# Optimization experiments

Hardware: AMD Instinct MI355X
Metric: run time of the kernel (lower is better)

Reference implementation:

```python
import jax, jax.numpy as jnp
import numpy as np

N = 8192
IN_F = 256
OUT_F = 128
ALPHA = 0.2
NEG = -9000000000000000.0

def setup_inputs() -> dict:
    key = jax.random.key(0)
    k1, k2, k3, k4 = jax.random.split(key, 4)
    h = jax.random.normal(k1, (N, IN_F), dtype=jnp.float32)
    adj = jax.random.randint(k2, (N, N), 0, 2, dtype=jnp.int32)
    # xavier-uniform-like params
    limW = float(np.sqrt(6.0 / (IN_F + OUT_F)))
    W = jax.random.uniform(k3, (IN_F, OUT_F), minval=-limW, maxval=limW, dtype=jnp.float32)
    lima = float(np.sqrt(6.0 / (2 * OUT_F + 1)))
    a = jax.random.uniform(k4, (2 * OUT_F, 1), minval=-lima, maxval=lima, dtype=jnp.float32)
    return {"h": h, "adj": adj, "W": W, "a": a}

def reference(h, adj, W, a):
    Wh = h @ W  # [N, F]
    # e_ij = LeakyReLU(a1.Wh_i + a2.Wh_j) -- avoids [N,N,2F] intermediate
    a1 = a[:OUT_F, 0]  # [F]
    a2 = a[OUT_F:, 0]  # [F]
    f1 = Wh @ a1  # [N]
    f2 = Wh @ a2  # [N]
    e = jax.nn.leaky_relu(f1[:, None] + f2[None, :], negative_slope=ALPHA)  # [N,N]
    att = jnp.where(adj > 0, e, jnp.float32(NEG))
    att = jax.nn.softmax(att, axis=1)
    h_prime = att @ Wh  # [N, F]
    return h_prime
```

## Files before the change

kernel.cpp:

```cpp
#include <hip/hip_runtime.h>
#include <hip/hip_bf16.h>

#define N    8192
#define INF  256
#define OUTF 128
#define ALPHA 0.2f
#define JS   8
#define NTS  (N / JS / 32)

typedef __attribute__((ext_vector_type(8))) short bf16x8;
typedef __attribute__((ext_vector_type(4))) float f32x4;

__device__ __forceinline__ unsigned short f2bf(float x) {
    union { float f; unsigned u; } v; v.f = x;
    unsigned r = v.u + 0x7fff + ((v.u >> 16) & 1);
    return (unsigned short)(r >> 16);
}

__device__ __forceinline__ void gll16(const void* g, void* l) {
    __builtin_amdgcn_global_load_lds(
        (const __attribute__((address_space(1))) unsigned*)g,
        (__attribute__((address_space(3))) unsigned*)l, 16, 0, 0);
}

__global__ __launch_bounds__(256) void k01_prep(
        const int* __restrict__ adj, unsigned* __restrict__ bits,
        const float* __restrict__ h, const float* __restrict__ W,
        const float* __restrict__ a,
        unsigned short* __restrict__ WhTb, float* __restrict__ f1, float* __restrict__ f2) {
    __shared__ float hs[8][INF];
    const int t = threadIdx.x;

    if (blockIdx.x >= 1024) {
        const size_t g = (size_t)(blockIdx.x - 1024) * 256 + t;
        const int4* p = (const int4*)adj + g * 8;
        unsigned b = 0;
        #pragma unroll
        for (int u = 0; u < 8; ++u) {
            int4 v = p[u];
            b |= (v.x > 0 ? 1u : 0u) << (u * 4 + 0);
            b |= (v.y > 0 ? 1u : 0u) << (u * 4 + 1);
            b |= (v.z > 0 ? 1u : 0u) << (u * 4 + 2);
            b |= (v.w > 0 ? 1u : 0u) << (u * 4 + 3);
        }
        bits[g] = b;
        return;
    }

    const int i0 = blockIdx.x * 8;
    #pragma unroll
    for (int u = 0; u < 2; ++u) {
        int idx = u * 256 + t;
        int r   = idx >> 6;
        int kq  = idx & 63;
        *(float4*)&hs[r][kq * 4] = *(const float4*)(h + (size_t)(i0 + r) * INF + kq * 4);
    }
    __syncthreads();

    const int rg = t >> 5;
    const int ct = t & 31;
    float acc[4] = {0.f, 0.f, 0.f, 0.f};

    #pragma unroll 8
    for (int k = 0; k < INF; ++k) {
        float4 wv = *(const float4*)(W + (size_t)k * OUTF + ct * 4);
        float  hx = hs[rg][k];
        acc[0] += hx * wv.x; acc[1] += hx * wv.y;
        acc[2] += hx * wv.z; acc[3] += hx * wv.w;
    }

    const int r0 = i0 + rg;
    const int jb = r0 >> 5;
    const int jo = r0 & 31;
    #pragma unroll
    for (int cc = 0; cc < 4; ++cc)
        WhTb[(size_t)jb * 4096 + (ct * 4 + cc) * 32 + jo] = f2bf(acc[cc]);

    const float4 a1v = *(const float4*)(a + ct * 4);
    const float4 a2v = *(const float4*)(a + OUTF + ct * 4);
    float p1 = acc[0]*a1v.x + acc[1]*a1v.y + acc[2]*a1v.z + acc[3]*a1v.w;
    float p2 = acc[0]*a2v.x + acc[1]*a2v.y + acc[2]*a2v.z + acc[3]*a2v.w;
    #pragma unroll
    for (int off = 16; off > 0; off >>= 1) {
        p1 += __shfl_down(p1, off, 32);
        p2 += __shfl_down(p2, off, 32);
    }
    if (ct == 0) { f1[r0] = p1; f2[r0] = p2; }
}

__device__ __forceinline__ float pbit(float f1r, float fv, unsigned byte_,
                                      int u, float& dsum) {
    float s = f1r + fv;
    float e = fmaxf(s, ALPHA * s);
    float p = (byte_ & (1u << u)) ? __expf(e) : 0.f;
    dsum += p;
    return p;
}

#define K2SUB(WORD, PH, JT)                                                  \
    {                                                                        \
        if ((JT) + 1 < NTS) {                                                \
            const char* ws_ = (const char*)WhTb + (size_t)(tile0 + (JT) + 1) * 8192; \
            char* bd_ = (char*)&bsm[(PH) ^ 1][0];                            \
            gll16(ws_ + t * 16,        bd_ + wv * 1024 + 0);                 \
            gll16(ws_ + 4096 + t * 16, bd_ + 4096 + wv * 1024 + 0);          \
        }                                                                    \
        float4 F0_ = *(const float4*)&f2s[(JT) * 32 + quad * 8];             \
        float4 F1_ = *(const float4*)&f2s[(JT) * 32 + quad * 8 + 4];         \
        unsigned byte_ = ((WORD) >> (quad << 3)) & 0xffu;                    \
        float p0_ = pbit(f1r, F0_.x, byte_, 0, dsum);                        \
        float p1_ = pbit(f1r, F0_.y, byte_, 1, dsum);                        \
        float p2_ = pbit(f1r, F0_.z, byte_, 2, dsum);                        \
        float p3_ = pbit(f1r, F0_.w, byte_, 3, dsum);                        \
        float p4_ = pbit(f1r, F1_.x, byte_, 4, dsum);                        \
        float p5_ = pbit(f1r, F1_.y, byte_, 5, dsum);                        \
        float p6_ = pbit(f1r, F1_.z, byte_, 6, dsum);                        \
        float p7_ = pbit(f1r, F1_.w, byte_, 7, dsum);                        \
        union { __hip_bfloat162 hh[4]; bf16x8 v; } pk_;                      \
        pk_.hh[0] = __float22bfloat162_rn(make_float2(p0_, p1_));            \
        pk_.hh[1] = __float22bfloat162_rn(make_float2(p2_, p3_));            \
        pk_.hh[2] = __float22bfloat162_rn(make_float2(p4_, p5_));            \
        pk_.hh[3] = __float22bfloat162_rn(make_float2(p6_, p7_));            \
        bf16x8 afrag = pk_.v;                                                \
        const char* bb_ = (const char*)&bsm[PH][0] + laneb2;                 \
        bf16x8 b0_ = *(const bf16x8*)(bb_);                                  \
        bf16x8 b1_ = *(const bf16x8*)(bb_ + 1024);                           \
        bf16x8 b2_ = *(const bf16x8*)(bb_ + 2048);                           \
        bf16x8 b3_ = *(const bf16x8*)(bb_ + 3072);                           \
        bf16x8 b4_ = *(const bf16x8*)(bb_ + 4096);                           \
        bf16x8 b5_ = *(const bf16x8*)(bb_ + 5120);                           \
        bf16x8 b6_ = *(const bf16x8*)(bb_ + 6144);                           \
        bf16x8 b7_ = *(const bf16x8*)(bb_ + 7168);                           \
        acc0 = __builtin_amdgcn_mfma_f32_16x16x32_bf16(afrag, b0_, acc0, 0, 0, 0); \
        acc1 = __builtin_amdgcn_mfma_f32_16x16x32_bf16(afrag, b1_, acc1, 0, 0, 0); \
        acc2 = __builtin_amdgcn_mfma_f32_16x16x32_bf16(afrag, b2_, acc2, 0, 0, 0); \
        acc3 = __builtin_amdgcn_mfma_f32_16x16x32_bf16(afrag, b3_, acc3, 0, 0, 0); \
        acc4 = __builtin_amdgcn_mfma_f32_16x16x32_bf16(afrag, b4_, acc4, 0, 0, 0); \
        acc5 = __builtin_amdgcn_mfma_f32_16x16x32_bf16(afrag, b5_, acc5, 0, 0, 0); \
        acc6 = __builtin_amdgcn_mfma_f32_16x16x32_bf16(afrag, b6_, acc6, 0, 0, 0); \
        acc7 = __builtin_amdgcn_mfma_f32_16x16x32_bf16(afrag, b7_, acc7, 0, 0, 0); \
        __syncthreads();                                                     \
    }

__global__ __launch_bounds__(256, 4) void k2_attn(
        const unsigned* __restrict__ bits, const unsigned short* __restrict__ WhTb,
        const float* __restrict__ f1, const float* __restrict__ f2,
        float* __restrict__ num, float* __restrict__ den) {
    __shared__ unsigned short bsm[2][4096];
    __shared__ float f2s[1024];

    const int t    = threadIdx.x;
    const int wv   = t >> 6;
    const int ln   = t & 63;
    const int m16  = ln & 15;
    const int quad = ln >> 4;
    const int i0   = blockIdx.x * 64;
    const int s    = blockIdx.y;
    const int row  = i0 + wv * 16 + m16;
    const int tile0 = s * NTS;
    const int j0    = s * (N / JS);
    const int laneb2 = (m16 * 32 + quad * 8) * 2;

    *(float4*)&f2s[t * 4] = *(const float4*)(f2 + j0 + t * 4);
    {
        const char* ws0 = (const char*)WhTb + (size_t)tile0 * 8192;
        char* bd = (char*)&bsm[0][0];
        gll16(ws0 + t * 16,        bd + wv * 1024);
        gll16(ws0 + 4096 + t * 16, bd + 4096 + wv * 1024);
    }

    const float f1r = f1[row];
    const uint4* brow = (const uint4*)(bits + (size_t)row * 256 + tile0);

    f32x4 acc0 = {0.f,0.f,0.f,0.f}, acc1 = {0.f,0.f,0.f,0.f};
    f32x4 acc2 = {0.f,0.f,0.f,0.f}, acc3 = {0.f,0.f,0.f,0.f};
    f32x4 acc4 = {0.f,0.f,0.f,0.f}, acc5 = {0.f,0.f,0.f,0.f};
    f32x4 acc6 = {0.f,0.f,0.f,0.f}, acc7 = {0.f,0.f,0.f,0.f};
    float dsum = 0.f;

    uint4 bwc = brow[0];
    __syncthreads();

    for (int g = 0; g < NTS / 4; ++g) {
        uint4 bwn = brow[(g + 1 < NTS / 4) ? g + 1 : g];
        const int jtb = g * 4;
        K2SUB(bwc.x, 0, jtb + 0)
        K2SUB(bwc.y, 1, jtb + 1)
        K2SUB(bwc.z, 0, jtb + 2)
        K2SUB(bwc.w, 1, jtb + 3)
        bwc = bwn;
    }

    dsum += __shfl_xor(dsum, 16);
    dsum += __shfl_xor(dsum, 32);
    if (quad == 0) den[(size_t)s * N + row] = dsum;

    float* np = num + (size_t)s * N * OUTF;
    #pragma unroll
    for (int r = 0; r < 4; ++r) {
        const size_t orow = (size_t)(i0 + wv * 16 + quad * 4 + r) * OUTF;
        np[orow + 0 * 16 + m16] = acc0[r];
        np[orow + 1 * 16 + m16] = acc1[r];
        np[orow + 2 * 16 + m16] = acc2[r];
        np[orow + 3 * 16 + m16] = acc3[r];
        np[orow + 4 * 16 + m16] = acc4[r];
        np[orow + 5 * 16 + m16] = acc5[r];
        np[orow + 6 * 16 + m16] = acc6[r];
        np[orow + 7 * 16 + m16] = acc7[r];
    }
}

__global__ __launch_bounds__(256) void k3_combine(
        const float* __restrict__ num, const float* __restrict__ den,
        float* __restrict__ out) {
    const int idx = blockIdx.x * 256 + threadIdx.x;
    const int row = idx >> 5;
    const int c4  = (idx & 31) * 4;
    float4 ns = {0.f,0.f,0.f,0.f};
    float  ds = 0.f;
    #pragma unroll
    for (int s = 0; s < JS; ++s) {
        float4 nv = *(const float4*)(num + ((size_t)s * N + row) * OUTF + c4);
        ns.x += nv.x; ns.y += nv.y; ns.z += nv.z; ns.w += nv.w;
        ds += den[(size_t)s * N + row];
    }
    const float inv = 1.0f / ds;
    float4 o = {ns.x * inv, ns.y * inv, ns.z * inv, ns.w * inv};
    *(float4*)(out + (size_t)row * OUTF + c4) = o;
}

extern "C" void kernel_launch(void* const* d_in, const int* in_sizes, int n_in,
                              void* d_out, int out_size, void* d_ws, size_t ws_size,
                              hipStream_t stream) {
    const float* h   = (const float*)d_in[0];
    const int*   adj = (const int*)  d_in[1];
    const float* W   = (const float*)d_in[2];
    const float* a   = (const float*)d_in[3];
    float* out = (float*)d_out;

    unsigned short* WhTb = (unsigned short*)d_ws;
    float*    f1   = (float*)(WhTb + (size_t)N * OUTF);
    float*    f2   = f1 + N;
    float*    den  = f2 + N;
    unsigned* bits = (unsigned*)(den + (size_t)JS * N);
    float*    num  = (float*)(bits + (size_t)N * (N / 32));

    k01_prep  <<<1024 + (N / 32) * (N / 256), 256, 0, stream>>>(adj, bits, h, W, a, WhTb, f1, f2);
    k2_attn   <<<dim3(N / 64, JS), 256, 0, stream>>>(bits, WhTb, f1, f2, num, den);
    k3_combine<<<(N * OUTF / 4) / 256, 256, 0, stream>>>(num, den, out);
}
```

Before: 431.4 us.

## Ballot-based adjacency bit packing and two-tile LDS pipeline stages in attention kernel

The adjacency packing now has each wavefront read coalesced 256-int rows and pack them with wave ballots. Previously each thread strided through 32 consecutive ints. The attention kernel now stages two Wh tiles per LDS buffer and synchronizes once per pair instead of once per tile, which halves the barriers and doubles the prefetch depth. This raises LDS use per block to about 36KB, which may limit occupancy.

```diff
diff --git a/kernel.cpp b/kernel.cpp
--- a/kernel.cpp
+++ b/kernel.cpp
@@ -32,18 +32,27 @@
     const int t = threadIdx.x;
 
     if (blockIdx.x >= 1024) {
-        const size_t g = (size_t)(blockIdx.x - 1024) * 256 + t;
-        const int4* p = (const int4*)adj + g * 8;
-        unsigned b = 0;
-        #pragma unroll
-        for (int u = 0; u < 8; ++u) {
-            int4 v = p[u];
-            b |= (v.x > 0 ? 1u : 0u) << (u * 4 + 0);
-            b |= (v.y > 0 ? 1u : 0u) << (u * 4 + 1);
-            b |= (v.z > 0 ? 1u : 0u) << (u * 4 + 2);
-            b |= (v.w > 0 ? 1u : 0u) << (u * 4 + 3);
+        const int pb = blockIdx.x - 1024;
+        const int w  = t >> 6;
+        const int ln = t & 63;
+        const size_t wi0 = ((size_t)pb * 4 + w) * 32;
+        #pragma unroll 2
+        for (int it = 0; it < 32; ++it) {
+            const size_t base = (wi0 + it) * 256;
+            int v0 = adj[base + ln];
+            int v1 = adj[base + 64 + ln];
+            int v2 = adj[base + 128 + ln];
+            int v3 = adj[base + 192 + ln];
+            unsigned long long b0 = __ballot(v0 > 0);
+            unsigned long long b1 = __ballot(v1 > 0);
+            unsigned long long b2 = __ballot(v2 > 0);
+            unsigned long long b3 = __ballot(v3 > 0);
+            if (ln < 8) {
+                int c = ln >> 1;
+                unsigned long long bb = (c == 0) ? b0 : (c == 1) ? b1 : (c == 2) ? b2 : b3;
+                bits[(wi0 + it) * 8 + ln] = (unsigned)(bb >> ((ln & 1) * 32));
+            }
         }
-        bits[g] = b;
         return;
     }
 
@@ -97,14 +106,8 @@
     return p;
 }
 
-#define K2SUB(WORD, PH, JT)                                                  \
+#define K2CMP(WORD, PH, SLOT, JT)                                            \
     {                                                                        \
-        if ((JT) + 1 < NTS) {                                                \
-            const char* ws_ = (const char*)WhTb + (size_t)(tile0 + (JT) + 1) * 8192; \
-            char* bd_ = (char*)&bsm[(PH) ^ 1][0];                            \
-            gll16(ws_ + t * 16,        bd_ + wv * 1024 + 0);                 \
-            gll16(ws_ + 4096 + t * 16, bd_ + 4096 + wv * 1024 + 0);          \
-        }                                                                    \
         float4 F0_ = *(const float4*)&f2s[(JT) * 32 + quad * 8];             \
         float4 F1_ = *(const float4*)&f2s[(JT) * 32 + quad * 8 + 4];         \
         unsigned byte_ = ((WORD) >> (quad << 3)) & 0xffu;                    \
@@ -122,7 +125,7 @@
         pk_.hh[2] = __float22bfloat162_rn(make_float2(p4_, p5_));            \
         pk_.hh[3] = __float22bfloat162_rn(make_float2(p6_, p7_));            \
         bf16x8 afrag = pk_.v;                                                \
-        const char* bb_ = (const char*)&bsm[PH][0] + laneb2;                 \
+        const char* bb_ = (const char*)&bsm[PH][(SLOT) * 4096] + laneb2;     \
         bf16x8 b0_ = *(const bf16x8*)(bb_);                                  \
         bf16x8 b1_ = *(const bf16x8*)(bb_ + 1024);                           \
         bf16x8 b2_ = *(const bf16x8*)(bb_ + 2048);                           \
@@ -139,6 +142,20 @@
         acc5 = __builtin_amdgcn_mfma_f32_16x16x32_bf16(afrag, b5_, acc5, 0, 0, 0); \
         acc6 = __builtin_amdgcn_mfma_f32_16x16x32_bf16(afrag, b6_, acc6, 0, 0, 0); \
         acc7 = __builtin_amdgcn_mfma_f32_16x16x32_bf16(afrag, b7_, acc7, 0, 0, 0); \
+    }
+
+#define K2PAIR(W0, W1, PH, JT)                                               \
+    {                                                                        \
+        if ((JT) + 2 < NTS) {                                                \
+            const char* ws_ = (const char*)WhTb + (size_t)(tile0 + (JT) + 2) * 8192; \
+            char* bd_ = (char*)&bsm[(PH) ^ 1][0];                            \
+            gll16(ws_ + t * 16,         bd_ + wv * 1024);                    \
+            gll16(ws_ + 4096 + t * 16,  bd_ + 4096 + wv * 1024);             \
+            gll16(ws_ + 8192 + t * 16,  bd_ + 8192 + wv * 1024);             \
+            gll16(ws_ + 12288 + t * 16, bd_ + 12288 + wv * 1024);            \
+        }                                                                    \
+        K2CMP(W0, PH, 0, JT)                                                 \
+        K2CMP(W1, PH, 1, (JT) + 1)                                           \
         __syncthreads();                                                     \
     }
 
@@ -146,7 +163,7 @@
         const unsigned* __restrict__ bits, const unsigned short* __restrict__ WhTb,
         const float* __restrict__ f1, const float* __restrict__ f2,
         float* __restrict__ num, float* __restrict__ den) {
-    __shared__ unsigned short bsm[2][4096];
+    __shared__ unsigned short bsm[2][8192];
     __shared__ float f2s[1024];
 
     const int t    = threadIdx.x;
@@ -165,8 +182,10 @@
     {
         const char* ws0 = (const char*)WhTb + (size_t)tile0 * 8192;
         char* bd = (char*)&bsm[0][0];
-        gll16(ws0 + t * 16,        bd + wv * 1024);
-        gll16(ws0 + 4096 + t * 16, bd + 4096 + wv * 1024);
+        gll16(ws0 + t * 16,         bd + wv * 1024);
+        gll16(ws0 + 4096 + t * 16,  bd + 4096 + wv * 1024);
+        gll16(ws0 + 8192 + t * 16,  bd + 8192 + wv * 1024);
+        gll16(ws0 + 12288 + t * 16, bd + 12288 + wv * 1024);
     }
 
     const float f1r = f1[row];
@@ -184,10 +203,8 @@
     for (int g = 0; g < NTS / 4; ++g) {
         uint4 bwn = brow[(g + 1 < NTS / 4) ? g + 1 : g];
         const int jtb = g * 4;
-        K2SUB(bwc.x, 0, jtb + 0)
-        K2SUB(bwc.y, 1, jtb + 1)
-        K2SUB(bwc.z, 0, jtb + 2)
-        K2SUB(bwc.w, 1, jtb + 3)
+        K2PAIR(bwc.x, bwc.y, 0, jtb)
+        K2PAIR(bwc.z, bwc.w, 1, jtb + 2)
         bwc = bwn;
     }
 
@@ -245,7 +262,7 @@
     unsigned* bits = (unsigned*)(den + (size_t)JS * N);
     float*    num  = (float*)(bits + (size_t)N * (N / 32));
 
-    k01_prep  <<<1024 + (N / 32) * (N / 256), 256, 0, stream>>>(adj, bits, h, W, a, WhTb, f1, f2);
+    k01_prep  <<<1024 + 2048, 256, 0, stream>>>(adj, bits, h, W, a, WhTb, f1, f2);
     k2_attn   <<<dim3(N / 64, JS), 256, 0, stream>>>(bits, WhTb, f1, f2, num, den);
     k3_combine<<<(N * OUTF / 4) / 256, 256, 0, stream>>>(num, den, out);
 }
```

New measurement: 439.1 us. No clear change (+1.8%).
